# Kernel tuning notes

Hardware: AMD Instinct MI355X
Metric: run time of the kernel (lower is better)

Reference implementation:

```python
import jax, jax.numpy as jnp
import numpy as np

N, S, L, E, H = 8, 2, 512, 1024, 16
D = E // H  # head_dim = 64


def setup_inputs() -> dict:
    key = jax.random.key(0)
    ks = jax.random.split(key, 10)
    inp = {
        "values": jax.random.normal(ks[0], (N, S, L, E), dtype=jnp.float32),
        "keys": jax.random.normal(ks[1], (N, S, L, E), dtype=jnp.float32),
        "query": jax.random.normal(ks[2], (N, S, L, E), dtype=jnp.float32),
        "mask": jax.random.randint(ks[3], (N, S, L, 1), 0, 2, dtype=jnp.int32),
        # per-head projection weights, nn.Linear(D, D, bias=False): y = x @ W.T
        "Wv": jax.random.normal(ks[4], (D, D), dtype=jnp.float32) / np.sqrt(D),
        "Wk": jax.random.normal(ks[5], (D, D), dtype=jnp.float32) / np.sqrt(D),
        "Wq": jax.random.normal(ks[6], (D, D), dtype=jnp.float32) / np.sqrt(D),
        # output projection nn.Linear(E, E)
        "Wo": jax.random.normal(ks[7], (E, E), dtype=jnp.float32) / np.sqrt(E),
        "bo": jax.random.normal(ks[8], (E,), dtype=jnp.float32) * 0.01,
    }
    return inp


def reference(values, keys, query, mask, Wv, Wk, Wq, Wo, bo):
    n, s, l, e = query.shape
    h, d = H, D
    key_len = keys.shape[2]
    # split heads: (n, s, len, h, d)
    v = values.reshape(n, s, l, h, d) @ Wv.T
    k = keys.reshape(n, s, l, h, d) @ Wk.T
    q = query.reshape(n, s, l, h, d) @ Wq.T
    # energy: (n, s, h, q_len, k_len)
    energy = jnp.einsum('nsqhd,nskhd->nshqk', q, k)
    # mask[:, :, :, 0] masks QUERY positions (broadcast over heads and k)
    m = mask[:, :, :, 0]  # (n, s, l)
    energy = jnp.where(m[:, :, None, :, None] == 0, jnp.float32(-1e20), energy)
    # NOTE: softmax over the QUERY axis (dim=3), faithful to the original
    attn = jax.nn.softmax(energy / jnp.sqrt(jnp.float32(key_len)), axis=3)
    out = jnp.einsum('nshql,nslhd->nsqhd', attn, v)
    out = out.reshape(n, s, l, h * d)
    return out @ Wo.T + bo
```

## Files before the change

kernel.cpp:

```cpp
#include <hip/hip_runtime.h>
#include <math.h>

#define LL 512
#define EE 1024
#define HH 16
#define DD 64
#define NSX 16
#define NT (NSX*LL)
#define NSLE (NT*EE)
#define SCALE_Q 0.06375871f

typedef unsigned short u16;
typedef short bf16x8 __attribute__((ext_vector_type(8)));
typedef float f32x4 __attribute__((ext_vector_type(4)));

__device__ inline u16 f2bf(float f) {
  unsigned u = __float_as_uint(f);
  u += 0x7fff + ((u >> 16) & 1);
  return (u16)(u >> 16);
}

#define FEXP2(x) __builtin_amdgcn_exp2f(x)
#define MFMA32(a, b, c) __builtin_amdgcn_mfma_f32_16x16x32_bf16((a), (b), (c), 0, 0, 0)

__device__ inline void gload16(const void* g, void* l) {
  __builtin_amdgcn_global_load_lds(
      (const __attribute__((address_space(1))) unsigned int*)g,
      (__attribute__((address_space(3))) unsigned int*)l, 16, 0, 0);
}

__global__ void __launch_bounds__(256) convw_kernel(
    const float* __restrict__ Wv, const float* __restrict__ Wk,
    const float* __restrict__ Wq, const float* __restrict__ Wo,
    u16* __restrict__ Wvb, u16* __restrict__ Wkb,
    u16* __restrict__ Wqb, u16* __restrict__ Wob) {
  int i = blockIdx.x * 256 + threadIdx.x;
  const float* s; u16* d; int j;
  if (i < 262144) { s = Wo; d = Wob; j = i; }
  else {
    j = i - 262144;
    if (j < 1024)      { s = Wv; d = Wvb; }
    else if (j < 2048) { s = Wk; d = Wkb; j -= 1024; }
    else               { s = Wq; d = Wqb; j -= 2048; }
  }
  float4 f = ((const float4*)s)[j];
  ushort4 o; o.x = f2bf(f.x); o.y = f2bf(f.y); o.z = f2bf(f.z); o.w = f2bf(f.w);
  ((ushort4*)d)[j] = o;
}

__global__ void __launch_bounds__(256) proj_kernel(
    const float* __restrict__ vals, const float* __restrict__ keys,
    const float* __restrict__ qry,
    const u16* __restrict__ Wvb, const u16* __restrict__ Wkb,
    const u16* __restrict__ Wqb,
    u16* __restrict__ vpT, u16* __restrict__ kp, u16* __restrict__ qp) {
  const int b = blockIdx.x;
  const int tt0 = b & 7, hg = (b >> 3) & 3, ns = (b >> 5) & 15, mat = b >> 9;
  const int tid = threadIdx.x;
  const int wid = tid >> 6, lane = tid & 63, quad = lane >> 4, l16 = lane & 15;
  const int h = hg*4 + wid;
  const float* src = (mat == 0 ? vals : mat == 1 ? keys : qry);
  const u16*   W   = (mat == 0 ? Wvb  : mat == 1 ? Wkb  : Wqb);
  u16* dst = (mat == 1 ? kp : qp);
  const float sc = (mat == 2) ? SCALE_Q : 1.f;
  float4 x[4][4];
  #pragma unroll
  for (int j = 0; j < 4; ++j) {
    const float* xr = src + (size_t)(ns*LL + (tt0 + 8*j)*16 + l16)*EE + h*DD;
    x[j][0] = *(const float4*)&xr[quad*8];
    x[j][1] = *(const float4*)&xr[quad*8 + 4];
    x[j][2] = *(const float4*)&xr[32 + quad*8];
    x[j][3] = *(const float4*)&xr[32 + quad*8 + 4];
  }
  bf16x8 wf[4][2];
  #pragma unroll
  for (int nt = 0; nt < 4; ++nt) {
    wf[nt][0] = *(const bf16x8*)&W[(nt*16 + l16)*DD + quad*8];
    wf[nt][1] = *(const bf16x8*)&W[(nt*16 + l16)*DD + 32 + quad*8];
  }
  f32x4 z = {0.f, 0.f, 0.f, 0.f};
  #pragma unroll
  for (int j = 0; j < 4; ++j) {
    const int tt = tt0 + 8*j;
    const int t0 = ns*LL + tt*16;
    bf16x8 af0, af1;
    af0[0] = (short)f2bf(x[j][0].x); af0[1] = (short)f2bf(x[j][0].y);
    af0[2] = (short)f2bf(x[j][0].z); af0[3] = (short)f2bf(x[j][0].w);
    af0[4] = (short)f2bf(x[j][1].x); af0[5] = (short)f2bf(x[j][1].y);
    af0[6] = (short)f2bf(x[j][1].z); af0[7] = (short)f2bf(x[j][1].w);
    af1[0] = (short)f2bf(x[j][2].x); af1[1] = (short)f2bf(x[j][2].y);
    af1[2] = (short)f2bf(x[j][2].z); af1[3] = (short)f2bf(x[j][2].w);
    af1[4] = (short)f2bf(x[j][3].x); af1[5] = (short)f2bf(x[j][3].y);
    af1[6] = (short)f2bf(x[j][3].z); af1[7] = (short)f2bf(x[j][3].w);
    if (mat == 0) {
      f32x4 acc[4];
      #pragma unroll
      for (int nt = 0; nt < 4; ++nt) {
        acc[nt] = MFMA32(af0, wf[nt][0], z);
        acc[nt] = MFMA32(af1, wf[nt][1], acc[nt]);
      }
      #pragma unroll
      for (int nt = 0; nt < 4; ++nt) {
        ushort4 o;
        o.x = f2bf(acc[nt][0]); o.y = f2bf(acc[nt][1]);
        o.z = f2bf(acc[nt][2]); o.w = f2bf(acc[nt][3]);
        size_t idx = ((size_t)((ns*HH + h)*DD + nt*16 + l16))*LL + tt*16 + quad*4;
        *(ushort4*)&vpT[idx] = o;
      }
    } else {
      f32x4 acc[4];
      #pragma unroll
      for (int nt = 0; nt < 4; ++nt) {
        acc[nt] = MFMA32(wf[nt][0], af0, z);
        acc[nt] = MFMA32(wf[nt][1], af1, acc[nt]);
      }
      #pragma unroll
      for (int nt = 0; nt < 4; ++nt) {
        ushort4 o;
        o.x = f2bf(acc[nt][0] * sc); o.y = f2bf(acc[nt][1] * sc);
        o.z = f2bf(acc[nt][2] * sc); o.w = f2bf(acc[nt][3] * sc);
        *(ushort4*)&dst[(size_t)(t0 + l16)*EE + h*DD + nt*16 + quad*4] = o;
      }
    }
  }
}

__global__ void __launch_bounds__(1024, 4) attn_kernel(
    const u16* __restrict__ qp, const u16* __restrict__ kp,
    const u16* __restrict__ vpT, const int* __restrict__ mask,
    u16* __restrict__ oat) {
  const int b = blockIdx.x;
  const int h = b & 15, ns = b >> 4;
  const int tid = threadIdx.x;
  const int wid = tid >> 6, lane = tid & 63, quad = lane >> 4, l16 = lane & 15;
  __shared__ u16 Ks[LL][72];
  __shared__ u16 Vt[2][DD][72];
  __shared__ u16 pt[16][32][40];
  __shared__ float csum[LL];
  float* psum = (float*)pt;
  const size_t vgbase = ((size_t)((ns*HH + h)*DD))*LL;
  const int vrow = tid >> 4, vseg = (tid & 15) * 4;
  ushort4 vreg = *(const ushort4*)&vpT[vgbase + (size_t)vrow*LL + vseg];
  const size_t kgbase = ((size_t)(ns*LL))*EE + h*DD;
  for (int i = tid; i < 4096; i += 1024) {
    int row = i >> 3, seg = (i & 7) * 8;
    *(bf16x8*)&Ks[row][seg] = *(const bf16x8*)&kp[kgbase + (size_t)row*EE + seg];
  }
  const int q0 = wid*32;
  bf16x8 qf[2][2];
  float maf[2][4];
  float mqf[2];
  #pragma unroll
  for (int qt = 0; qt < 2; ++qt) {
    const u16* qrow = qp + ((size_t)(ns*LL + q0 + qt*16 + l16))*EE + h*DD;
    qf[qt][0] = *(const bf16x8*)&qrow[quad*8];
    qf[qt][1] = *(const bf16x8*)&qrow[32 + quad*8];
    #pragma unroll
    for (int r = 0; r < 4; ++r)
      maf[qt][r] = mask[ns*LL + q0 + qt*16 + quad*4 + r] ? 1.f : 0.f;
    mqf[qt] = mask[ns*LL + q0 + qt*16 + l16] ? 1.f : 0.f;
  }
  f32x4 z = {0.f, 0.f, 0.f, 0.f};
  __syncthreads();
  for (int lt = 0; lt < 32; ++lt) {
    bf16x8 kf0 = *(const bf16x8*)&Ks[lt*16 + l16][quad*8];
    bf16x8 kf1 = *(const bf16x8*)&Ks[lt*16 + l16][32 + quad*8];
    float part = 0.f;
    #pragma unroll
    for (int qt = 0; qt < 2; ++qt) {
      f32x4 e = MFMA32(qf[qt][0], kf0, z);
      e = MFMA32(qf[qt][1], kf1, e);
      #pragma unroll
      for (int r = 0; r < 4; ++r)
        part += maf[qt][r] * FEXP2(e[r]);
    }
    part += __shfl_xor(part, 16);
    part += __shfl_xor(part, 32);
    if (quad == 0) psum[wid*512 + lt*16 + l16] = part;
  }
  __syncthreads();
  if (tid < LL) {
    float s = 0.f;
    #pragma unroll
    for (int w = 0; w < 16; ++w) s += psum[w*512 + tid];
    csum[tid] = (s > 0.f) ? 1.f/s : 0.f;
  }
  __syncthreads();
  *(ushort4*)&Vt[0][vrow][vseg] = vreg;
  f32x4 acc[4][2] = {{z,z},{z,z},{z,z},{z,z}};
  for (int lc = 0; lc < 8; ++lc) {
    ushort4 nreg;
    if (lc < 7)
      nreg = *(const ushort4*)&vpT[vgbase + (size_t)vrow*LL + (lc+1)*64 + vseg];
    __syncthreads();
    #pragma unroll
    for (int lt2 = 0; lt2 < 4; ++lt2) {
      const int lb = lc*64 + lt2*16;
      bf16x8 kf0 = *(const bf16x8*)&Ks[lb + l16][quad*8];
      bf16x8 kf1 = *(const bf16x8*)&Ks[lb + l16][32 + quad*8];
      float4 cs4 = *(const float4*)&csum[lb + quad*4];
      #pragma unroll
      for (int qt = 0; qt < 2; ++qt) {
        f32x4 e = MFMA32(kf0, qf[qt][0], z);
        e = MFMA32(kf1, qf[qt][1], e);
        const float m = mqf[qt];
        ushort4 o;
        o.x = f2bf(m * cs4.x * FEXP2(e[0]));
        o.y = f2bf(m * cs4.y * FEXP2(e[1]));
        o.z = f2bf(m * cs4.z * FEXP2(e[2]));
        o.w = f2bf(m * cs4.w * FEXP2(e[3]));
        *(ushort4*)&pt[wid][qt*16 + l16][(lt2 & 1)*16 + quad*4] = o;
      }
      if (lt2 & 1) {
        bf16x8 vb[4];
        #pragma unroll
        for (int dt = 0; dt < 4; ++dt)
          vb[dt] = *(const bf16x8*)&Vt[lc & 1][dt*16 + l16]
                                      [(lt2 >> 1)*32 + quad*8];
        #pragma unroll
        for (int qt = 0; qt < 2; ++qt) {
          bf16x8 pa = *(const bf16x8*)&pt[wid][qt*16 + l16][quad*8];
          #pragma unroll
          for (int dt = 0; dt < 4; ++dt)
            acc[dt][qt] = MFMA32(pa, vb[dt], acc[dt][qt]);
        }
      }
    }
    if (lc < 7)
      *(ushort4*)&Vt[(lc+1) & 1][vrow][vseg] = nreg;
  }
  #pragma unroll
  for (int qt = 0; qt < 2; ++qt)
    #pragma unroll
    for (int dt = 0; dt < 4; ++dt)
      #pragma unroll
      for (int r = 0; r < 4; ++r)
        oat[((size_t)(ns*LL + q0 + qt*16 + quad*4 + r))*EE + h*DD + dt*16 + l16] =
            f2bf(acc[dt][qt][r]);
}

__global__ void __launch_bounds__(256) out_gemm_kernel(
    const u16* __restrict__ A, const u16* __restrict__ Wob,
    const float* __restrict__ bo, float* __restrict__ Y) {
  __shared__ u16 As[128][64];
  __shared__ u16 Bs[64][64];
  const int b = blockIdx.x;
  const int nb = b & 15, mb = b >> 4;
  const int m0 = mb*128, n0 = nb*64;
  const int tid = threadIdx.x;
  const int wid = tid >> 6, lane = tid & 63, quad = lane >> 4, l16 = lane & 15;
  const int wm = (wid >> 1)*64, wn = (wid & 1)*32;
  const int r0 = tid >> 3, sseg = (tid & 7) * 8;
  u16* adst = &As[0][0] + tid*8;
  u16* bdst = &Bs[0][0] + tid*8;
  f32x4 z = {0.f, 0.f, 0.f, 0.f};
  f32x4 acc[4][2];
  #pragma unroll
  for (int i = 0; i < 4; ++i)
    #pragma unroll
    for (int j = 0; j < 2; ++j) acc[i][j] = z;
  for (int k0 = 0; k0 < EE; k0 += 64) {
    __syncthreads();
    #pragma unroll
    for (int it = 0; it < 4; ++it)
      gload16(&A[(size_t)(m0 + it*32 + r0)*EE + k0 + sseg], adst + it*2048);
    #pragma unroll
    for (int it = 0; it < 2; ++it)
      gload16(&Wob[(size_t)(n0 + it*32 + r0)*EE + k0 + sseg], bdst + it*2048);
    __syncthreads();
    #pragma unroll
    for (int kk = 0; kk < 2; ++kk) {
      bf16x8 af[4], bfr[2];
      #pragma unroll
      for (int i = 0; i < 4; ++i)
        af[i] = *(const bf16x8*)&As[wm + i*16 + l16][kk*32 + quad*8];
      #pragma unroll
      for (int j = 0; j < 2; ++j)
        bfr[j] = *(const bf16x8*)&Bs[wn + j*16 + l16][kk*32 + quad*8];
      #pragma unroll
      for (int i = 0; i < 4; ++i)
        #pragma unroll
        for (int j = 0; j < 2; ++j)
          acc[i][j] = MFMA32(af[i], bfr[j], acc[i][j]);
    }
  }
  #pragma unroll
  for (int i = 0; i < 4; ++i)
    #pragma unroll
    for (int j = 0; j < 2; ++j) {
      int col = n0 + wn + j*16 + l16;
      float bias = bo[col];
      #pragma unroll
      for (int r = 0; r < 4; ++r)
        Y[(size_t)(m0 + wm + i*16 + quad*4 + r)*EE + col] = acc[i][j][r] + bias;
    }
}

extern "C" void kernel_launch(void* const* d_in, const int* in_sizes, int n_in,
                              void* d_out, int out_size, void* d_ws, size_t ws_size,
                              hipStream_t stream) {
  const float* values = (const float*)d_in[0];
  const float* keysp  = (const float*)d_in[1];
  const float* query  = (const float*)d_in[2];
  const int*   mask   = (const int*)d_in[3];
  const float* Wv = (const float*)d_in[4];
  const float* Wk = (const float*)d_in[5];
  const float* Wq = (const float*)d_in[6];
  const float* Wo = (const float*)d_in[7];
  const float* bo = (const float*)d_in[8];
  float* Y = (float*)d_out;

  u16* qp  = (u16*)d_ws;
  u16* kp  = qp + NSLE;
  u16* vpT = kp + NSLE;
  u16* oat = vpT + NSLE;
  u16* Wob = oat + NSLE;
  u16* Wvb = Wob + EE*EE;
  u16* Wkb = Wvb + DD*DD;
  u16* Wqb = Wkb + DD*DD;

  convw_kernel<<<1036, 256, 0, stream>>>(Wv, Wk, Wq, Wo, Wvb, Wkb, Wqb, Wob);
  proj_kernel<<<3*NSX*4*8, 256, 0, stream>>>(values, keysp, query,
                                             Wvb, Wkb, Wqb, vpT, kp, qp);
  attn_kernel<<<NSX*HH, 1024, 0, stream>>>(qp, kp, vpT, mask, oat);
  out_gemm_kernel<<<(NT/128)*(EE/64), 256, 0, stream>>>(oat, Wob, bo, Y);
}
```

Baseline: 232.8 us.

## Stage projection input rows through shared memory with coalesced full-row loads

The projection kernel now assigns each block a 16-token tile covering all 16 heads. It loads full 1024-float rows with coalesced float4 loads, converts them to bf16 into an LDS buffer in a software-pipelined loop, and then has each wave read its MFMA fragments for 4 heads from LDS. Previously each lane did strided 32-byte loads per head across separate blocks. This is meant to improve global-memory coalescing on the bandwidth-bound fp32 input read, at the cost of about 33KB of LDS per block, a barrier, and fewer, larger blocks (1536 instead of 1536, with a different mapping) plus a launch-bounds occupancy hint.

```diff
diff --git a/kernel.cpp b/kernel.cpp
--- a/kernel.cpp
+++ b/kernel.cpp
@@ -48,50 +48,61 @@
   ((ushort4*)d)[j] = o;
 }
 
-__global__ void __launch_bounds__(256) proj_kernel(
+__global__ void __launch_bounds__(256, 4) proj_kernel(
     const float* __restrict__ vals, const float* __restrict__ keys,
     const float* __restrict__ qry,
     const u16* __restrict__ Wvb, const u16* __restrict__ Wkb,
     const u16* __restrict__ Wqb,
     u16* __restrict__ vpT, u16* __restrict__ kp, u16* __restrict__ qp) {
   const int b = blockIdx.x;
-  const int tt0 = b & 7, hg = (b >> 3) & 3, ns = (b >> 5) & 15, mat = b >> 9;
+  const int tile = b & 31, ns = (b >> 5) & 15, mat = b >> 9;
   const int tid = threadIdx.x;
   const int wid = tid >> 6, lane = tid & 63, quad = lane >> 4, l16 = lane & 15;
-  const int h = hg*4 + wid;
   const float* src = (mat == 0 ? vals : mat == 1 ? keys : qry);
   const u16*   W   = (mat == 0 ? Wvb  : mat == 1 ? Wkb  : Wqb);
   u16* dst = (mat == 1 ? kp : qp);
   const float sc = (mat == 2) ? SCALE_Q : 1.f;
-  float4 x[4][4];
-  #pragma unroll
-  for (int j = 0; j < 4; ++j) {
-    const float* xr = src + (size_t)(ns*LL + (tt0 + 8*j)*16 + l16)*EE + h*DD;
-    x[j][0] = *(const float4*)&xr[quad*8];
-    x[j][1] = *(const float4*)&xr[quad*8 + 4];
-    x[j][2] = *(const float4*)&xr[32 + quad*8];
-    x[j][3] = *(const float4*)&xr[32 + quad*8 + 4];
-  }
+  __shared__ u16 Xs[16][1032];
+  const int t0 = ns*LL + tile*16;
+  const float* gbase = src + (size_t)t0*EE;
+  float4 xb0[4], xb1[4];
+  #pragma unroll
+  for (int k = 0; k < 4; ++k)
+    xb0[k] = *(const float4*)&gbase[(size_t)k*EE + tid*4];
+  #pragma unroll
+  for (int k = 0; k < 4; ++k)
+    xb1[k] = *(const float4*)&gbase[(size_t)(4 + k)*EE + tid*4];
   bf16x8 wf[4][2];
   #pragma unroll
   for (int nt = 0; nt < 4; ++nt) {
     wf[nt][0] = *(const bf16x8*)&W[(nt*16 + l16)*DD + quad*8];
     wf[nt][1] = *(const bf16x8*)&W[(nt*16 + l16)*DD + 32 + quad*8];
   }
+  #pragma unroll
+  for (int bt = 0; bt < 4; ++bt) {
+    float4 nx[4];
+    if (bt < 2) {
+      #pragma unroll
+      for (int k = 0; k < 4; ++k)
+        nx[k] = *(const float4*)&gbase[(size_t)((bt + 2)*4 + k)*EE + tid*4];
+    }
+    #pragma unroll
+    for (int k = 0; k < 4; ++k) {
+      ushort4 o;
+      o.x = f2bf(xb0[k].x); o.y = f2bf(xb0[k].y);
+      o.z = f2bf(xb0[k].z); o.w = f2bf(xb0[k].w);
+      *(ushort4*)&Xs[bt*4 + k][tid*4] = o;
+    }
+    #pragma unroll
+    for (int k = 0; k < 4; ++k) { xb0[k] = xb1[k]; if (bt < 2) xb1[k] = nx[k]; }
+  }
   f32x4 z = {0.f, 0.f, 0.f, 0.f};
-  #pragma unroll
-  for (int j = 0; j < 4; ++j) {
-    const int tt = tt0 + 8*j;
-    const int t0 = ns*LL + tt*16;
-    bf16x8 af0, af1;
-    af0[0] = (short)f2bf(x[j][0].x); af0[1] = (short)f2bf(x[j][0].y);
-    af0[2] = (short)f2bf(x[j][0].z); af0[3] = (short)f2bf(x[j][0].w);
-    af0[4] = (short)f2bf(x[j][1].x); af0[5] = (short)f2bf(x[j][1].y);
-    af0[6] = (short)f2bf(x[j][1].z); af0[7] = (short)f2bf(x[j][1].w);
-    af1[0] = (short)f2bf(x[j][2].x); af1[1] = (short)f2bf(x[j][2].y);
-    af1[2] = (short)f2bf(x[j][2].z); af1[3] = (short)f2bf(x[j][2].w);
-    af1[4] = (short)f2bf(x[j][3].x); af1[5] = (short)f2bf(x[j][3].y);
-    af1[6] = (short)f2bf(x[j][3].z); af1[7] = (short)f2bf(x[j][3].w);
+  __syncthreads();
+  #pragma unroll
+  for (int ht = 0; ht < 4; ++ht) {
+    const int h = wid*4 + ht;
+    bf16x8 af0 = *(const bf16x8*)&Xs[l16][h*DD + quad*8];
+    bf16x8 af1 = *(const bf16x8*)&Xs[l16][h*DD + 32 + quad*8];
     if (mat == 0) {
       f32x4 acc[4];
       #pragma unroll
@@ -104,7 +115,7 @@
         ushort4 o;
         o.x = f2bf(acc[nt][0]); o.y = f2bf(acc[nt][1]);
         o.z = f2bf(acc[nt][2]); o.w = f2bf(acc[nt][3]);
-        size_t idx = ((size_t)((ns*HH + h)*DD + nt*16 + l16))*LL + tt*16 + quad*4;
+        size_t idx = ((size_t)((ns*HH + h)*DD + nt*16 + l16))*LL + tile*16 + quad*4;
         *(ushort4*)&vpT[idx] = o;
       }
     } else {
@@ -320,8 +331,8 @@
   u16* Wqb = Wkb + DD*DD;
 
   convw_kernel<<<1036, 256, 0, stream>>>(Wv, Wk, Wq, Wo, Wvb, Wkb, Wqb, Wob);
-  proj_kernel<<<3*NSX*4*8, 256, 0, stream>>>(values, keysp, query,
-                                             Wvb, Wkb, Wqb, vpT, kp, qp);
+  proj_kernel<<<3*NSX*32, 256, 0, stream>>>(values, keysp, query,
+                                            Wvb, Wkb, Wqb, vpT, kp, qp);
   attn_kernel<<<NSX*HH, 1024, 0, stream>>>(qp, kp, vpT, mask, oat);
   out_gemm_kernel<<<(NT/128)*(EE/64), 256, 0, stream>>>(oat, Wob, bo, Y);
 }
```

New measurement: 234.0 us. No clear change (+0.5%).
